# Kernel tuning notes

Hardware: AMD Instinct MI355X
Metric: run time of the kernel (lower is better)

## Reference

```python
import jax, jax.numpy as jnp
import numpy as np

# ---- static config (matches init_kwargs) ----
B, N, D, FH, FW, C = 2, 6, 48, 16, 44, 80
OGH, OGW, DOWNSAMPLE = 256, 704, 16
D_MIN, D_MAX = 2.0, 58.0
XB = (-51.2, 51.2, 0.4); YB = (-51.2, 51.2, 0.4); ZB = (-10.0, 10.0, 20.0)
NX, NY, NZ = 256, 256, 1  # (ub-lb)/step per bound
DX = jnp.array([XB[2], YB[2], ZB[2]], jnp.float32)
LOWER = jnp.array([XB[0], YB[0], ZB[0]], jnp.float32)  # bx - dx/2


def _frustum():
    # UD depth discretization: d_i = d_min + i*(d_max-d_min)/D
    ds = D_MIN + (D_MAX - D_MIN) / D * np.arange(D, dtype=np.float32)
    ds = np.broadcast_to(ds[:, None, None], (D, FH, FW))
    xs = np.broadcast_to(np.linspace(0, OGW - 1, FW, dtype=np.float32)[None, None, :], (D, FH, FW))
    ys = np.broadcast_to(np.linspace(0, OGH - 1, FH, dtype=np.float32)[None, :, None], (D, FH, FW))
    return jnp.asarray(np.stack([xs, ys, ds], -1))  # [D,FH,FW,3]

FRUSTUM = _frustum()


def setup_inputs() -> dict:
    key = jax.random.key(0)
    k1, k2 = jax.random.split(key)
    x = jax.random.normal(k1, (B, N, D, FH, FW, C), dtype=jnp.float32)
    # camera-to-ego rotation: ego_x = z_cam (fwd), ego_y = -x_cam, ego_z = -y_cam
    R = np.array([[0.0, 0.0, 1.0], [-1.0, 0.0, 0.0], [0.0, -1.0, 0.0]], np.float32)
    rots = jnp.asarray(np.broadcast_to(R, (B, N, 3, 3)).copy())
    trans = 2.0 * jax.random.normal(k2, (B, N, 3), dtype=jnp.float32)
    K = np.array([[500.0, 0.0, OGW / 2.0], [0.0, 500.0, OGH / 2.0], [0.0, 0.0, 1.0]], np.float32)
    intrins = jnp.asarray(np.broadcast_to(K, (B, N, 3, 3)).copy())
    post_rots = jnp.asarray(np.broadcast_to(np.eye(3, dtype=np.float32), (B, N, 3, 3)).copy())
    post_trans = jnp.zeros((B, N, 3), jnp.float32)
    return {"x": x, "rots": rots, "trans": trans, "intrins": intrins,
            "post_rots": post_rots, "post_trans": post_trans}


def _get_geometry(rots, trans, intrins, post_rots, post_trans):
    # frustum -> ego-frame 3D points: [B,N,D,FH,FW,3]
    pts = FRUSTUM[None, None] - post_trans[:, :, None, None, None, :]
    inv_post = jnp.linalg.inv(post_rots)
    pts = jnp.einsum('bnij,bndhwj->bndhwi', inv_post, pts)
    # un-normalize pixel coords by depth
    pts = jnp.concatenate([pts[..., :2] * pts[..., 2:3], pts[..., 2:3]], axis=-1)
    combine = jnp.einsum('bnij,bnjk->bnik', rots, jnp.linalg.inv(intrins))
    pts = jnp.einsum('bnij,bndhwj->bndhwi', combine, pts)
    return pts + trans[:, :, None, None, None, :]


def _voxel_pooling(geom, x):
    Nprime = B * N * D * FH * FW
    xf = x.reshape(Nprime, C)
    # voxel indices; torch .long() truncates toward zero -> astype matches
    gi = ((geom.reshape(Nprime, 3) - LOWER) / DX).astype(jnp.int32)
    batch_ix = jnp.repeat(jnp.arange(B, dtype=jnp.int32), Nprime // B)
    kept = ((gi[:, 0] >= 0) & (gi[:, 0] < NX) &
            (gi[:, 1] >= 0) & (gi[:, 1] < NY) &
            (gi[:, 2] >= 0) & (gi[:, 2] < NZ))
    gi = jnp.where(kept[:, None], gi, 0)
    # flat index into (B, NZ, NY, NX); equivalent aggregation to sort+quickcumsum
    flat = ((batch_ix * NZ + gi[:, 2]) * NY + gi[:, 1]) * NX + gi[:, 0]
    xm = jnp.where(kept[:, None], xf, 0.0)
    pooled = jax.ops.segment_sum(xm, flat, num_segments=B * NZ * NY * NX)
    final = pooled.reshape(B, NZ, NY, NX, C).transpose(0, 4, 1, 2, 3)
    return final  # [B, C, NZ, NY, NX]


def reference(x, rots, trans, intrins, post_rots, post_trans):
    geom = _get_geometry(rots, trans, intrins, post_rots, post_trans)
    return _voxel_pooling(geom, x)
```

## Files before the change

### kernel.cpp

```cpp
#include <hip/hip_runtime.h>


#define NCH       80
#define GRID_HW   65536
#define OUT_PER_B 5242880
#define HSTRIDE   3520
#define PTS_PER_BN 33792

#define N_ENT_MAX 405504
#define P_BYTES   129761280u
#define NEXT_OFF  129761280u
#define HEAD_OFF  131383296u
#define CNT_OFF   131907584u
#define META_OFF  131907840u
#define WS_NEED   133529856u

__device__ inline void inv3(const double a[9], double inv[9]) {
    double c00 =  a[4]*a[8] - a[5]*a[7];
    double c01 = -(a[3]*a[8] - a[5]*a[6]);
    double c02 =  a[3]*a[7] - a[4]*a[6];
    double det = a[0]*c00 + a[1]*c01 + a[2]*c02;
    double id  = 1.0/det;
    inv[0] = c00*id;
    inv[1] = (a[2]*a[7]-a[1]*a[8])*id;
    inv[2] = (a[1]*a[5]-a[2]*a[4])*id;
    inv[3] = c01*id;
    inv[4] = (a[0]*a[8]-a[2]*a[6])*id;
    inv[5] = (a[2]*a[3]-a[0]*a[5])*id;
    inv[6] = c02*id;
    inv[7] = (a[1]*a[6]-a[0]*a[7])*id;
    inv[8] = (a[0]*a[4]-a[1]*a[3])*id;
}

__device__ inline void prep_bn(const float* __restrict__ rots,
                               const float* __restrict__ trans,
                               const float* __restrict__ intrins,
                               const float* __restrict__ post_rots,
                               const float* __restrict__ post_trans,
                               int bn, double* o) {
    double pr[9], kk[9], rt[9], ipr[9], ik[9];
    #pragma unroll
    for (int i = 0; i < 9; i++) {
        pr[i] = (double)post_rots[bn*9 + i];
        kk[i] = (double)intrins[bn*9 + i];
        rt[i] = (double)rots[bn*9 + i];
    }
    inv3(pr, ipr);
    inv3(kk, ik);
    #pragma unroll
    for (int i = 0; i < 9; i++) o[i] = ipr[i];
    #pragma unroll
    for (int r = 0; r < 3; r++)
        #pragma unroll
        for (int c = 0; c < 3; c++)
            o[9 + r*3 + c] = rt[r*3+0]*ik[0*3+c] + rt[r*3+1]*ik[1*3+c] + rt[r*3+2]*ik[2*3+c];
    #pragma unroll
    for (int i = 0; i < 3; i++) o[18 + i] = (double)post_trans[bn*3 + i];
    #pragma unroll
    for (int i = 0; i < 3; i++) o[21 + i] = (double)trans[bn*3 + i];
}

__global__ void prep_kernel(const float* __restrict__ rots,
                            const float* __restrict__ trans,
                            const float* __restrict__ intrins,
                            const float* __restrict__ post_rots,
                            const float* __restrict__ post_trans,
                            double* __restrict__ tw) {
    int bn = threadIdx.x;
    if (bn >= 12) return;
    prep_bn(rots, trans, intrins, post_rots, post_trans, bn, tw + bn*24);
}

__global__ __launch_bounds__(256) void zero_kernel(float4* __restrict__ p, int n4) {
    int i = blockIdx.x * 256 + threadIdx.x;
    int stride = gridDim.x * 256;
    for (; i < n4; i += stride) p[i] = make_float4(0.f, 0.f, 0.f, 0.f);
}

__global__ __launch_bounds__(256) void init_heads(int* __restrict__ head, int* __restrict__ counter) {
    int i = blockIdx.x * 256 + threadIdx.x;
    if (i < 131072) head[i] = -1;
    if (i == 0) counter[0] = 0;
}

__device__ inline void geom_points(const double* __restrict__ t,
                                   int b, int d, int tid, int* s_base) {
    const float dsv = __fadd_rn(2.0f, __fmul_rn((float)(56.0 / 48.0), (float)d));
    for (int idx = tid; idx < 704; idx += 256) {
        const int h = idx / 44;
        const int w = idx - h * 44;
        float xsv = (w == 43) ? 703.0f : (float)((double)w * (703.0 / 43.0));
        float ysv = (float)(h * 17);

        double px = (double)xsv - t[18];
        double py = (double)ysv - t[19];
        double pz = (double)dsv - t[20];
        double q0 = t[0]*px + t[1]*py + t[2]*pz;
        double q1 = t[3]*px + t[4]*py + t[5]*pz;
        double q2 = t[6]*px + t[7]*py + t[8]*pz;
        q0 *= q2;
        q1 *= q2;
        double e0 = t[9]*q0  + t[10]*q1 + t[11]*q2 + t[21];
        double e1 = t[12]*q0 + t[13]*q1 + t[14]*q2 + t[22];
        double e2 = t[15]*q0 + t[16]*q1 + t[17]*q2 + t[23];

        const double lxy = (double)(-51.2f);
        const double dxy = (double)(0.4f);
        int gx = (int)((e0 - lxy) / dxy);
        int gy = (int)((e1 - lxy) / dxy);
        int gz = (int)((e2 - (double)(-10.0f)) / (double)(20.0f));
        int base = -1;
        if (gx >= 0 && gx < 256 && gy >= 0 && gy < 256 && gz == 0)
            base = (b << 16) | (gy << 8) | gx;
        s_base[idx] = base;
    }
}

__global__ __launch_bounds__(256) void geom_groups(const float* __restrict__ rots,
                                                   const float* __restrict__ trans,
                                                   const float* __restrict__ intrins,
                                                   const float* __restrict__ post_rots,
                                                   const float* __restrict__ post_trans,
                                                   int* __restrict__ nxt,
                                                   int* __restrict__ head,
                                                   int* __restrict__ counter,
                                                   unsigned* __restrict__ ent_meta) {
    __shared__ double   s_t[24];
    __shared__ int      s_base[704];
    __shared__ int      s_gbase[704];
    __shared__ unsigned s_gmask[704];
    __shared__ int      s_gcount[44];
    __shared__ int      s_goff[44];
    __shared__ int      s_eb;

    const int tid   = threadIdx.x;
    const int slice = blockIdx.x;
    const int bn    = slice / 48;
    const int d     = slice - bn * 48;
    const int b     = bn / 6;

    if (tid == 0)
        prep_bn(rots, trans, intrins, post_rots, post_trans, bn, s_t);
    __syncthreads();

    geom_points(s_t, b, d, tid, s_base);
    __syncthreads();

    if (tid < 44) {
        int gb[16]; unsigned gm[16];
        int cnt = 0;
        #pragma unroll
        for (int h = 0; h < 16; h++) {
            int pb = s_base[h * 44 + tid];
            if (pb >= 0) {
                int j = 0;
                for (; j < cnt; j++) if (gb[j] == pb) break;
                if (j < cnt) gm[j] |= (1u << h);
                else { gb[cnt] = pb; gm[cnt] = (1u << h); cnt++; }
            }
        }
        s_gcount[tid] = cnt;
        for (int j = 0; j < cnt; j++) {
            s_gbase[tid * 16 + j] = gb[j];
            s_gmask[tid * 16 + j] = gm[j];
        }
    }
    __syncthreads();

    if (tid == 0) {
        int off = 0;
        for (int w = 0; w < 44; w++) { s_goff[w] = off; off += s_gcount[w]; }
        s_eb = atomicAdd(counter, off);
    }
    __syncthreads();

    if (tid < 44) {
        int off = s_goff[tid];
        int cnt = s_gcount[tid];
        for (int k = 0; k < cnt; k++) {
            int e = s_eb + off + k;
            ent_meta[e] = ((unsigned)slice << 22) | ((unsigned)tid << 16)
                        | (s_gmask[tid * 16 + k] & 0xFFFFu);
            nxt[e] = atomicExch(&head[s_gbase[tid * 16 + k]], e);
        }
    }
}

__global__ __launch_bounds__(256) void reduce_kernel(const float* __restrict__ x,
                                                     const unsigned* __restrict__ ent_meta,
                                                     const int* __restrict__ counter,
                                                     float* __restrict__ P) {
    const int NE = counter[0];
    const int total = NE * 20;
    int i = blockIdx.x * 256 + threadIdx.x;
    const int stride = gridDim.x * 256;
    for (; i < total; i += stride) {
        int e  = i / 20;
        int c4 = i - e * 20;
        unsigned meta = ent_meta[e];
        int slice   = (int)(meta >> 22);
        int w       = (int)((meta >> 16) & 63u);
        unsigned mm = meta & 0xFFFFu;
        const float* xb = x + (size_t)(slice * 704 + w) * NCH + c4 * 4;
        float ax = 0.f, ay = 0.f, az = 0.f, aw = 0.f;
        #pragma unroll
        for (int h = 0; h < 16; h++) {
            float4 v = *(const float4*)(xb + h * HSTRIDE);
            float m = (float)((mm >> h) & 1u);
            ax = fmaf(m, v.x, ax);
            ay = fmaf(m, v.y, ay);
            az = fmaf(m, v.z, az);
            aw = fmaf(m, v.w, aw);
        }
        float4 r; r.x = ax; r.y = ay; r.z = az; r.w = aw;
        *(float4*)(P + (size_t)e * NCH + c4 * 4) = r;
    }
}

__global__ __launch_bounds__(256) void gather_kernel(const float* __restrict__ P,
                                                     const int* __restrict__ nxt,
                                                     const int* __restrict__ head,
                                                     float* __restrict__ out) {
    __shared__ float tile[64 * 81];
    __shared__ int   s_head[64];
    const int tid = threadIdx.x;
    const int b   = blockIdx.x >> 10;
    const int v0  = (blockIdx.x & 1023) * 64;
    if (tid < 64) s_head[tid] = head[(b << 16) + v0 + tid];
    __syncthreads();
    for (int i = 0; i < 20; i++) {
        int j = i * 256 + tid;
        int v = j / 80;
        int c = j - v * 80;
        float s = 0.f;
        int e = s_head[v];
        while (e >= 0) {
            s += P[(size_t)e * NCH + c];
            e = nxt[e];
        }
        tile[v * 81 + c] = s;
    }
    __syncthreads();
    float* dst = out + (size_t)b * OUT_PER_B + v0;
    #pragma unroll
    for (int i = 0; i < 20; i++) {
        int k  = i * 256 + tid;
        int c  = k >> 6;
        int lv = k & 63;
        dst[(size_t)c * GRID_HW + lv] = tile[lv * 81 + c];
    }
}

__global__ __launch_bounds__(256) void scatter_direct_kernel(const float* __restrict__ x,
                                                             const double* __restrict__ ws,
                                                             float* __restrict__ out) {
    __shared__ int      s_base[704];
    __shared__ int      s_colbase[44];
    __shared__ unsigned s_mask[44];
    __shared__ unsigned s_fb[44];

    const int tid = threadIdx.x;
    const int bn  = blockIdx.x / 48;
    const int d   = blockIdx.x - bn * 48;
    const int b   = bn / 6;
    geom_points(ws + bn * 24, b, d, tid, s_base);
    __syncthreads();

    if (tid < 44) {
        int cb = -1; unsigned mm = 0, fb = 0;
        #pragma unroll
        for (int h = 0; h < 16; h++) {
            int pb = s_base[h * 44 + tid];
            if (pb >= 0) {
                if (cb < 0) cb = pb;
                if (pb == cb) mm |= (1u << h);
                else          fb |= (1u << h);
            }
        }
        s_colbase[tid] = cb;
        s_mask[tid]    = mm;
        s_fb[tid]      = fb;
    }
    __syncthreads();

    const float* xb0 = x + ((size_t)bn * PTS_PER_BN + (size_t)d * 704) * NCH;
    #pragma unroll
    for (int pass = 0; pass < 4; pass++) {
        int item = pass * 256 + tid;
        if (item >= 880) break;
        int w  = item / 20;
        int c4 = item - w * 20;
        unsigned mm = s_mask[w];
        unsigned fb = s_fb[w];
        if (!(mm | fb)) continue;
        const float* xb = xb0 + (size_t)w * NCH + c4 * 4;
        float ax = 0.f, ay = 0.f, az = 0.f, aw = 0.f;
        #pragma unroll
        for (int h = 0; h < 16; h++) {
            if ((mm >> h) & 1u) {
                float4 v = *(const float4*)(xb + h * HSTRIDE);
                ax += v.x; ay += v.y; az += v.z; aw += v.w;
            } else if ((fb >> h) & 1u) {
                float4 v = *(const float4*)(xb + h * HSTRIDE);
                int vb = s_base[h * 44 + w];
                float* o = out + (size_t)(vb >> 16) * OUT_PER_B + (vb & 65535);
                atomicAdd(o + (size_t)(c4*4 + 0) * GRID_HW, v.x);
                atomicAdd(o + (size_t)(c4*4 + 1) * GRID_HW, v.y);
                atomicAdd(o + (size_t)(c4*4 + 2) * GRID_HW, v.z);
                atomicAdd(o + (size_t)(c4*4 + 3) * GRID_HW, v.w);
            }
        }
        if (mm) {
            int vb = s_colbase[w];
            float* o = out + (size_t)(vb >> 16) * OUT_PER_B + (vb & 65535);
            atomicAdd(o + (size_t)(c4*4 + 0) * GRID_HW, ax);
            atomicAdd(o + (size_t)(c4*4 + 1) * GRID_HW, ay);
            atomicAdd(o + (size_t)(c4*4 + 2) * GRID_HW, az);
            atomicAdd(o + (size_t)(c4*4 + 3) * GRID_HW, aw);
        }
    }
}

extern "C" void kernel_launch(void* const* d_in, const int* in_sizes, int n_in,
                              void* d_out, int out_size, void* d_ws, size_t ws_size,
                              hipStream_t stream) {
    const float* x          = (const float*)d_in[0];
    const float* rots       = (const float*)d_in[1];
    const float* trans      = (const float*)d_in[2];
    const float* intrins    = (const float*)d_in[3];
    const float* post_rots  = (const float*)d_in[4];
    const float* post_trans = (const float*)d_in[5];
    float* out = (float*)d_out;

    if (ws_size >= (size_t)WS_NEED) {
        float*    P       = (float*)d_ws;
        int*      nxt     = (int*)((char*)d_ws + NEXT_OFF);
        int*      head    = (int*)((char*)d_ws + HEAD_OFF);
        int*      counter = (int*)((char*)d_ws + CNT_OFF);
        unsigned* meta    = (unsigned*)((char*)d_ws + META_OFF);
        init_heads<<<512, 256, 0, stream>>>(head, counter);
        geom_groups<<<576, 256, 0, stream>>>(rots, trans, intrins,
                                             post_rots, post_trans,
                                             nxt, head, counter, meta);
        reduce_kernel<<<2048, 256, 0, stream>>>(x, meta, counter, P);
        gather_kernel<<<2048, 256, 0, stream>>>(P, nxt, head, out);
    } else if (ws_size >= 12 * 24 * sizeof(double)) {
        double* tw = (double*)d_ws;
        zero_kernel<<<2560, 256, 0, stream>>>((float4*)out, out_size / 16);
        prep_kernel<<<1, 64, 0, stream>>>(rots, trans, intrins, post_rots, post_trans, tw);
        scatter_direct_kernel<<<576, 256, 0, stream>>>(x, tw, out);
    }
}
```

Before: 240.4 us.

## Fuse column reduction into per-voxel gather, drop intermediate partial-sum buffer

Removes the reduce_kernel that wrote per-entry 80-channel partial sums to a large workspace buffer. The gather kernel now walks each voxel's linked list, caches up to 32 entry ids in shared memory, and reads x directly with float4 loads, accumulating in double. This avoids writing and re-reading about 130 MB of intermediate data and one kernel launch. In exchange, voxels with long lists are processed serially per thread, which can cause load imbalance, and the double accumulation adds conversion cost.

Result: slower. 261.6 us (+8.8%).

```diff
diff --git a/kernel.cpp b/kernel.cpp
--- a/kernel.cpp
+++ b/kernel.cpp
@@ -6,14 +6,14 @@
 #define OUT_PER_B 5242880
 #define HSTRIDE   3520
 #define PTS_PER_BN 33792
+#define CAP       32
 
 #define N_ENT_MAX 405504
-#define P_BYTES   129761280u
-#define NEXT_OFF  129761280u
-#define HEAD_OFF  131383296u
-#define CNT_OFF   131907584u
-#define META_OFF  131907840u
-#define WS_NEED   133529856u
+#define NEXT_OFF  0u
+#define HEAD_OFF  1622016u
+#define CNT_OFF   2146304u
+#define META_OFF  2146560u
+#define WS_NEED   3768576u
 
 __device__ inline void inv3(const double a[9], double inv[9]) {
     double c00 =  a[4]*a[8] - a[5]*a[7];
@@ -91,7 +91,6 @@
         const int w = idx - h * 44;
         float xsv = (w == 43) ? 703.0f : (float)((double)w * (703.0 / 43.0));
         float ysv = (float)(h * 17);
-
         double px = (double)xsv - t[18];
         double py = (double)ysv - t[19];
         double pz = (double)dsv - t[20];
@@ -103,7 +102,6 @@
         double e0 = t[9]*q0  + t[10]*q1 + t[11]*q2 + t[21];
         double e1 = t[12]*q0 + t[13]*q1 + t[14]*q2 + t[22];
         double e2 = t[15]*q0 + t[16]*q1 + t[17]*q2 + t[23];
-
         const double lxy = (double)(-51.2f);
         const double dxy = (double)(0.4f);
         int gx = (int)((e0 - lxy) / dxy);
@@ -186,61 +184,69 @@
     }
 }
 
-__global__ __launch_bounds__(256) void reduce_kernel(const float* __restrict__ x,
-                                                     const unsigned* __restrict__ ent_meta,
-                                                     const int* __restrict__ counter,
-                                                     float* __restrict__ P) {
-    const int NE = counter[0];
-    const int total = NE * 20;
-    int i = blockIdx.x * 256 + threadIdx.x;
-    const int stride = gridDim.x * 256;
-    for (; i < total; i += stride) {
-        int e  = i / 20;
-        int c4 = i - e * 20;
-        unsigned meta = ent_meta[e];
-        int slice   = (int)(meta >> 22);
-        int w       = (int)((meta >> 16) & 63u);
-        unsigned mm = meta & 0xFFFFu;
-        const float* xb = x + (size_t)(slice * 704 + w) * NCH + c4 * 4;
-        float ax = 0.f, ay = 0.f, az = 0.f, aw = 0.f;
-        #pragma unroll
-        for (int h = 0; h < 16; h++) {
-            float4 v = *(const float4*)(xb + h * HSTRIDE);
-            float m = (float)((mm >> h) & 1u);
-            ax = fmaf(m, v.x, ax);
-            ay = fmaf(m, v.y, ay);
-            az = fmaf(m, v.z, az);
-            aw = fmaf(m, v.w, aw);
-        }
-        float4 r; r.x = ax; r.y = ay; r.z = az; r.w = aw;
-        *(float4*)(P + (size_t)e * NCH + c4 * 4) = r;
-    }
-}
-
-__global__ __launch_bounds__(256) void gather_kernel(const float* __restrict__ P,
-                                                     const int* __restrict__ nxt,
-                                                     const int* __restrict__ head,
-                                                     float* __restrict__ out) {
+__device__ inline void entry_accum(const float* __restrict__ x, unsigned m, int c4,
+                                   double& dx, double& dy, double& dz, double& dw) {
+    int slice   = (int)(m >> 22);
+    int w       = (int)((m >> 16) & 63u);
+    unsigned mm = m & 0xFFFFu;
+    const float* xb = x + (size_t)(slice * 704 + w) * NCH + c4 * 4;
+    float ax = 0.f, ay = 0.f, az = 0.f, aw = 0.f;
+    #pragma unroll
+    for (int h = 0; h < 16; h++) {
+        float4 v = *(const float4*)(xb + h * HSTRIDE);
+        float mk = (float)((mm >> h) & 1u);
+        ax = fmaf(mk, v.x, ax);
+        ay = fmaf(mk, v.y, ay);
+        az = fmaf(mk, v.z, az);
+        aw = fmaf(mk, v.w, aw);
+    }
+    dx += (double)ax; dy += (double)ay; dz += (double)az; dw += (double)aw;
+}
+
+__global__ __launch_bounds__(256, 4) void gather_direct(const float* __restrict__ x,
+                                                        const int* __restrict__ nxt,
+                                                        const int* __restrict__ head,
+                                                        const unsigned* __restrict__ ent_meta,
+                                                        float* __restrict__ out) {
     __shared__ float tile[64 * 81];
-    __shared__ int   s_head[64];
+    __shared__ int   s_ent[64 * CAP];
+    __shared__ int   s_cnt[64];
+    __shared__ int   s_ovf[64];
+
     const int tid = threadIdx.x;
     const int b   = blockIdx.x >> 10;
     const int v0  = (blockIdx.x & 1023) * 64;
-    if (tid < 64) s_head[tid] = head[(b << 16) + v0 + tid];
-    __syncthreads();
-    for (int i = 0; i < 20; i++) {
-        int j = i * 256 + tid;
-        int v = j / 80;
-        int c = j - v * 80;
-        float s = 0.f;
-        int e = s_head[v];
+
+    if (tid < 64) {
+        int e = head[(b << 16) + v0 + tid];
+        int c = 0;
+        while (e >= 0 && c < CAP) { s_ent[tid * CAP + c] = e; c++; e = nxt[e]; }
+        s_cnt[tid] = c;
+        s_ovf[tid] = e;
+    }
+    __syncthreads();
+
+    #pragma unroll
+    for (int i = 0; i < 5; i++) {
+        int j  = i * 256 + tid;
+        int v  = j / 20;
+        int c4 = j - v * 20;
+        double dx = 0.0, dy = 0.0, dz = 0.0, dw = 0.0;
+        const int cnt = s_cnt[v];
+        for (int k = 0; k < cnt; k++)
+            entry_accum(x, ent_meta[s_ent[v * CAP + k]], c4, dx, dy, dz, dw);
+        int e = s_ovf[v];
         while (e >= 0) {
-            s += P[(size_t)e * NCH + c];
+            entry_accum(x, ent_meta[e], c4, dx, dy, dz, dw);
             e = nxt[e];
         }
-        tile[v * 81 + c] = s;
-    }
-    __syncthreads();
+        tile[v * 81 + c4 * 4 + 0] = (float)dx;
+        tile[v * 81 + c4 * 4 + 1] = (float)dy;
+        tile[v * 81 + c4 * 4 + 2] = (float)dz;
+        tile[v * 81 + c4 * 4 + 3] = (float)dw;
+    }
+    __syncthreads();
+
     float* dst = out + (size_t)b * OUT_PER_B + v0;
     #pragma unroll
     for (int i = 0; i < 20; i++) {
@@ -333,7 +339,6 @@
     float* out = (float*)d_out;
 
     if (ws_size >= (size_t)WS_NEED) {
-        float*    P       = (float*)d_ws;
         int*      nxt     = (int*)((char*)d_ws + NEXT_OFF);
         int*      head    = (int*)((char*)d_ws + HEAD_OFF);
         int*      counter = (int*)((char*)d_ws + CNT_OFF);
@@ -342,8 +347,7 @@
         geom_groups<<<576, 256, 0, stream>>>(rots, trans, intrins,
                                              post_rots, post_trans,
                                              nxt, head, counter, meta);
-        reduce_kernel<<<2048, 256, 0, stream>>>(x, meta, counter, P);
-        gather_kernel<<<2048, 256, 0, stream>>>(P, nxt, head, out);
+        gather_direct<<<2048, 256, 0, stream>>>(x, nxt, head, meta, out);
     } else if (ws_size >= 12 * 24 * sizeof(double)) {
         double* tw = (double*)d_ws;
         zero_kernel<<<2560, 256, 0, stream>>>((float4*)out, out_size / 16);
```

## Prefetch linked-list entries into shared memory and gather with float4 loads

Applied to the files above, without the earlier changes.

The gather kernel now has 64 threads walk each voxel's linked list once and cache up to 32 entry indices in shared memory. All threads then sum P rows with float4 loads instead of each thread re-walking the list through dependent nxt loads for one scalar channel. Lists longer than the cap continue through a fallback walk. Accumulation switches to double precision, which on MI355X costs extra FP64 work and register pressure, while launch bounds request higher occupancy.

Measured after the change: 229.9 us. 1.05x faster.

```diff
diff --git a/kernel.cpp b/kernel.cpp
--- a/kernel.cpp
+++ b/kernel.cpp
@@ -6,6 +6,7 @@
 #define OUT_PER_B 5242880
 #define HSTRIDE   3520
 #define PTS_PER_BN 33792
+#define CAP       32
 
 #define N_ENT_MAX 405504
 #define P_BYTES   129761280u
@@ -91,7 +92,6 @@
         const int w = idx - h * 44;
         float xsv = (w == 43) ? 703.0f : (float)((double)w * (703.0 / 43.0));
         float ysv = (float)(h * 17);
-
         double px = (double)xsv - t[18];
         double py = (double)ysv - t[19];
         double pz = (double)dsv - t[20];
@@ -103,7 +103,6 @@
         double e0 = t[9]*q0  + t[10]*q1 + t[11]*q2 + t[21];
         double e1 = t[12]*q0 + t[13]*q1 + t[14]*q2 + t[22];
         double e2 = t[15]*q0 + t[16]*q1 + t[17]*q2 + t[23];
-
         const double lxy = (double)(-51.2f);
         const double dxy = (double)(0.4f);
         int gx = (int)((e0 - lxy) / dxy);
@@ -217,30 +216,52 @@
     }
 }
 
-__global__ __launch_bounds__(256) void gather_kernel(const float* __restrict__ P,
-                                                     const int* __restrict__ nxt,
-                                                     const int* __restrict__ head,
-                                                     float* __restrict__ out) {
+__global__ __launch_bounds__(256, 4) void gather_tiled(const float* __restrict__ P,
+                                                       const int* __restrict__ nxt,
+                                                       const int* __restrict__ head,
+                                                       float* __restrict__ out) {
     __shared__ float tile[64 * 81];
-    __shared__ int   s_head[64];
+    __shared__ int   s_ent[64 * CAP];
+    __shared__ int   s_cnt[64];
+    __shared__ int   s_ovf[64];
+
     const int tid = threadIdx.x;
     const int b   = blockIdx.x >> 10;
     const int v0  = (blockIdx.x & 1023) * 64;
-    if (tid < 64) s_head[tid] = head[(b << 16) + v0 + tid];
-    __syncthreads();
-    for (int i = 0; i < 20; i++) {
-        int j = i * 256 + tid;
-        int v = j / 80;
-        int c = j - v * 80;
-        float s = 0.f;
-        int e = s_head[v];
+
+    if (tid < 64) {
+        int e = head[(b << 16) + v0 + tid];
+        int c = 0;
+        while (e >= 0 && c < CAP) { s_ent[tid * CAP + c] = e; c++; e = nxt[e]; }
+        s_cnt[tid] = c;
+        s_ovf[tid] = e;
+    }
+    __syncthreads();
+
+    #pragma unroll
+    for (int i = 0; i < 5; i++) {
+        int j  = i * 256 + tid;
+        int v  = j / 20;
+        int c4 = j - v * 20;
+        double dx = 0.0, dy = 0.0, dz = 0.0, dw = 0.0;
+        const int cnt = s_cnt[v];
+        for (int k = 0; k < cnt; k++) {
+            const float4 p = *(const float4*)(P + (size_t)s_ent[v * CAP + k] * NCH + c4 * 4);
+            dx += (double)p.x; dy += (double)p.y; dz += (double)p.z; dw += (double)p.w;
+        }
+        int e = s_ovf[v];
         while (e >= 0) {
-            s += P[(size_t)e * NCH + c];
+            const float4 p = *(const float4*)(P + (size_t)e * NCH + c4 * 4);
+            dx += (double)p.x; dy += (double)p.y; dz += (double)p.z; dw += (double)p.w;
             e = nxt[e];
         }
-        tile[v * 81 + c] = s;
-    }
-    __syncthreads();
+        tile[v * 81 + c4 * 4 + 0] = (float)dx;
+        tile[v * 81 + c4 * 4 + 1] = (float)dy;
+        tile[v * 81 + c4 * 4 + 2] = (float)dz;
+        tile[v * 81 + c4 * 4 + 3] = (float)dw;
+    }
+    __syncthreads();
+
     float* dst = out + (size_t)b * OUT_PER_B + v0;
     #pragma unroll
     for (int i = 0; i < 20; i++) {
@@ -343,7 +364,7 @@
                                              post_rots, post_trans,
                                              nxt, head, counter, meta);
         reduce_kernel<<<2048, 256, 0, stream>>>(x, meta, counter, P);
-        gather_kernel<<<2048, 256, 0, stream>>>(P, nxt, head, out);
+        gather_tiled<<<2048, 256, 0, stream>>>(P, nxt, head, out);
     } else if (ws_size >= 12 * 24 * sizeof(double)) {
         double* tw = (double*)d_ws;
         zero_kernel<<<2560, 256, 0, stream>>>((float4*)out, out_size / 16);
```
